# Performance work log

Measured on AMD Instinct MI355X. Metric: run time of the kernel, lower is better.

The kernel has to match this reference:

```python
import jax, jax.numpy as jnp
import numpy as np

NUM_HEADS = 8
BN_EPS = 1e-5


def _conv3x3(x, w, B, N, s):
    # x: (B, N, 3*s*s). Torch loops conv2d per batch element; equivalent to one
    # conv over the flattened (B*N, 3, s, s) batch.
    xi = x.reshape(B * N, 3, s, s)
    y = jax.lax.conv_general_dilated(
        xi, w, window_strides=(1, 1), padding='SAME',
        dimension_numbers=('NCHW', 'OIHW', 'NCHW'))
    return y.reshape(B, N, 3 * s * s)


def setup_inputs() -> dict:
    key = jax.random.key(0)
    ks = jax.random.split(key, 8)
    B, N, C, s = 4, 1024, 768, 16
    H = NUM_HEADS
    q = jax.random.normal(ks[0], (B, N, C), jnp.float32)
    k = jax.random.normal(ks[1], (B, N, C), jnp.float32)
    v = jax.random.normal(ks[2], (B, N, C), jnp.float32)
    qw = jax.random.normal(ks[3], (3, 3, 3, 3), jnp.float32) * 0.1
    kw = jax.random.normal(ks[4], (3, 3, 3, 3), jnp.float32) * 0.1
    vw = jax.random.normal(ks[5], (3, 3, 3, 3), jnp.float32) * 0.1
    rw = jax.random.normal(ks[6], (H, H), jnp.float32) * 0.3  # Conv2d(H,H,1,1) weight
    rb = jnp.zeros((H,), jnp.float32)
    bn_gamma = jnp.ones((H,), jnp.float32)
    bn_beta = jnp.zeros((H,), jnp.float32)
    pw = jax.random.normal(ks[7], (C, C), jnp.float32) * 0.02
    pb = jnp.zeros((C,), jnp.float32)
    return dict(q=q, k=k, v=v, qw=qw, kw=kw, vw=vw, rw=rw, rb=rb,
                bn_gamma=bn_gamma, bn_beta=bn_beta, pw=pw, pb=pb)


def reference(q, k, v, qw, kw, vw, rw, rb, bn_gamma, bn_beta, pw, pb):
    B, N, C = q.shape
    H = NUM_HEADS
    d = C // H
    s = int(np.sqrt(C // 3))
    scale = d ** -0.5
    # conv-projected q/k/v, back to (B, N, C)
    qc = _conv3x3(q, qw, B, N, s)
    kc = _conv3x3(k, kw, B, N, s)
    vc = _conv3x3(v, vw, B, N, s)
    # split heads: (B, H, N, d)
    qh = qc.reshape(B, N, H, d).transpose(0, 2, 1, 3)
    kh = kc.reshape(B, N, H, d).transpose(0, 2, 1, 3)
    vh = vc.reshape(B, N, H, d).transpose(0, 2, 1, 3)
    attn = jax.nn.softmax(jnp.einsum('bhnd,bhmd->bhnm', qh, kh) * scale, axis=-1)
    # re-attention: 1x1 cross-head conv + BatchNorm2d(H) in eval mode
    # (running_mean=0, running_var=1); reatten_scale = 1.0
    attn = jnp.einsum('bhnm,gh->bgnm', attn, rw) + rb[None, :, None, None]
    attn = attn * (bn_gamma / jnp.sqrt(1.0 + BN_EPS))[None, :, None, None] \
           + bn_beta[None, :, None, None]
    x = jnp.einsum('bhnm,bhmd->bhnd', attn, vh)
    x = x.transpose(0, 2, 1, 3).reshape(B, N, C)
    return x @ pw.T + pb
```

## Files before the change

kernel.cpp:

```cpp
#include <hip/hip_runtime.h>
#include <hip/hip_bf16.h>
#include <math.h>

#define B 4
#define N 1024
#define C 768
#define H 8
#define D 96

typedef _Float16 half8 __attribute__((ext_vector_type(8)));
typedef _Float16 half4 __attribute__((ext_vector_type(4)));
typedef float f32x4 __attribute__((ext_vector_type(4)));

#define BN_RSQ 0.9999950000374997f
#define QK_SCALE 0.10206207261596577f

__global__ __launch_bounds__(256) void conv_tok(const float* __restrict__ x,
                                                const float* __restrict__ w,
                                                _Float16* __restrict__ out) {
    __shared__ float sx[768];
    __shared__ float sw[81];
    int t = blockIdx.x;
    const float* xt = x + (size_t)t * 768;
    int tid = threadIdx.x;
    sx[tid]       = xt[tid];
    sx[tid + 256] = xt[tid + 256];
    sx[tid + 512] = xt[tid + 512];
    if (tid < 81) sw[tid] = w[tid];
    __syncthreads();
    int i = tid >> 4, j = tid & 15;
    float acc0 = 0.f, acc1 = 0.f, acc2 = 0.f;
    #pragma unroll
    for (int c = 0; c < 3; ++c) {
        #pragma unroll
        for (int di = 0; di < 3; ++di) {
            int ii = i + di - 1;
            if (ii < 0 || ii > 15) continue;
            #pragma unroll
            for (int dj = 0; dj < 3; ++dj) {
                int jj = j + dj - 1;
                if (jj < 0 || jj > 15) continue;
                float xv = sx[c * 256 + ii * 16 + jj];
                acc0 += xv * sw[(0 * 3 + c) * 9 + di * 3 + dj];
                acc1 += xv * sw[(1 * 3 + c) * 9 + di * 3 + dj];
                acc2 += xv * sw[(2 * 3 + c) * 9 + di * 3 + dj];
            }
        }
    }
    _Float16* ot = out + (size_t)t * 768;
    ot[0 * 256 + tid] = (_Float16)acc0;
    ot[1 * 256 + tid] = (_Float16)acc1;
    ot[2 * 256 + tid] = (_Float16)acc2;
}

__global__ __launch_bounds__(256) void transpose_v(const _Float16* __restrict__ vcH,
                                                   _Float16* __restrict__ vcT) {
    __shared__ _Float16 tile[64][66];
    int n0 = blockIdx.x * 64, c0 = blockIdx.y * 64, b = blockIdx.z;
    int tid = threadIdx.x;
    for (int i = tid; i < 4096; i += 256) {
        int r = i >> 6, c = i & 63;
        tile[r][c] = vcH[((size_t)(b * N + n0 + r)) * C + c0 + c];
    }
    __syncthreads();
    for (int i = tid; i < 4096; i += 256) {
        int cr = i >> 6, nc = i & 63;
        vcT[((size_t)(b * 768 + c0 + cr)) * N + n0 + nc] = tile[nc][cr];
    }
}

__global__ __launch_bounds__(256) void vsum_part(const _Float16* __restrict__ vcH,
                                                 float* __restrict__ vsum) {
    int col = blockIdx.x * 256 + threadIdx.x;
    int b = col / 768, c = col - b * 768;
    int m0 = blockIdx.y * 64;
    float s = 0.f;
    #pragma unroll 8
    for (int m = 0; m < 64; ++m)
        s += (float)vcH[((size_t)(b * N) + m0 + m) * C + c];
    atomicAdd(&vsum[b * 768 + c], s);
}

__global__ __launch_bounds__(256) void qk_mfma(const _Float16* __restrict__ qcH,
                                               const _Float16* __restrict__ kcH,
                                               _Float16* __restrict__ expS,
                                               float* __restrict__ Lrow) {
    __shared__ _Float16 Qt[128 * 96];
    __shared__ _Float16 Kt[128 * 96];
    const int n0 = blockIdx.x * 128, m0 = blockIdx.y * 128, z = blockIdx.z;
    const int b = z >> 3, h = z & 7;
    const int tid = threadIdx.x;
    const _Float16* qg = qcH + ((size_t)(b * N + n0)) * C + h * D;
    const _Float16* kg = kcH + ((size_t)(b * N + m0)) * C + h * D;
    char* Qb = (char*)Qt;
    char* Kb = (char*)Kt;
    #pragma unroll
    for (int it = 0; it < 6; ++it) {
        int chunk = it * 256 + tid;
        int r = chunk / 12, cc = (chunk - r * 12) * 8;
        half8 qv = *(const half8*)(qg + (size_t)r * C + cc);
        half8 kv = *(const half8*)(kg + (size_t)r * C + cc);
        int off = ((r * 96 + cc) * 2) ^ ((r & 7) << 4);
        *(half8*)(Qb + off) = qv;
        *(half8*)(Kb + off) = kv;
    }
    __syncthreads();
    const int wid = tid >> 6, lane = tid & 63;
    const int wr = wid >> 1, wc = wid & 1;
    const int l15 = lane & 15, l4 = lane >> 4;
    f32x4 acc[4][4] = {};
    #pragma unroll
    for (int ks = 0; ks < 3; ++ks) {
        int k0 = ks * 32 + l4 * 8;
        half8 a[4], bf[4];
        #pragma unroll
        for (int fm = 0; fm < 4; ++fm) {
            int row = wr * 64 + fm * 16 + l15;
            a[fm] = *(half8*)(Qb + (((row * 96 + k0) * 2) ^ ((row & 7) << 4)));
        }
        #pragma unroll
        for (int fn = 0; fn < 4; ++fn) {
            int row = wc * 64 + fn * 16 + l15;
            bf[fn] = *(half8*)(Kb + (((row * 96 + k0) * 2) ^ ((row & 7) << 4)));
        }
        #pragma unroll
        for (int fm = 0; fm < 4; ++fm)
            #pragma unroll
            for (int fn = 0; fn < 4; ++fn)
                acc[fm][fn] = __builtin_amdgcn_mfma_f32_16x16x32_f16(a[fm], bf[fn], acc[fm][fn], 0, 0, 0);
    }
    #pragma unroll
    for (int fm = 0; fm < 4; ++fm) {
        #pragma unroll
        for (int j = 0; j < 4; ++j) {
            int row = n0 + wr * 64 + fm * 16 + l4 * 4 + j;
            float rs = 0.f;
            #pragma unroll
            for (int fn = 0; fn < 4; ++fn) {
                float p = __expf(acc[fm][fn][j] * QK_SCALE);
                rs += p;
                int m = m0 + wc * 64 + fn * 16 + l15;
                expS[((size_t)z * N + row) * N + m] = (_Float16)p;
            }
            rs += __shfl_xor(rs, 1);
            rs += __shfl_xor(rs, 2);
            rs += __shfl_xor(rs, 4);
            rs += __shfl_xor(rs, 8);
            if (l15 == 0) atomicAdd(&Lrow[z * N + row], rs);
        }
    }
}

__global__ __launch_bounds__(512, 2) void pv_fused(const _Float16* __restrict__ expS,
                                                   const float* __restrict__ Lrow,
                                                   const _Float16* __restrict__ vcT,
                                                   const float* __restrict__ rw,
                                                   const float* __restrict__ gamma,
                                                   float* __restrict__ x) {
    __shared__ _Float16 AL[8 * 64 * 32];
    __shared__ _Float16 VL[8 * 96 * 32];
    __shared__ float w2s[64];
    const int n0 = blockIdx.x * 64;
    const int mbase = blockIdx.y * 256;
    const int b = blockIdx.z;
    const int tid = threadIdx.x;
    if (tid < 64) {
        int g = tid >> 3, hh = tid & 7;
        w2s[tid] = gamma[g] * BN_RSQ * rw[g * 8 + hh];
    }
    const int n_t = tid >> 3;
    const int mq = (tid & 7) * 4;
    float IL[8];
    #pragma unroll
    for (int h = 0; h < 8; ++h)
        IL[h] = 1.0f / Lrow[(b * 8 + h) * N + n0 + n_t];
    __syncthreads();
    const int wid = tid >> 6, lane = tid & 63;
    const int l15 = lane & 15, l4 = lane >> 4;
    char* ALb = (char*)AL;
    char* VLb = (char*)VL;
    f32x4 acc[4][6] = {};
    for (int msub = 0; msub < 8; ++msub) {
        const int m0 = mbase + msub * 32;
        half4 sE[8];
        #pragma unroll
        for (int h = 0; h < 8; ++h)
            sE[h] = *(const half4*)(expS + ((size_t)(b * 8 + h) * N + n0 + n_t) * N + m0 + mq);
        half8 vv[6];
        int voff[6];
        #pragma unroll
        for (int it = 0; it < 6; ++it) {
            int q = it * 512 + tid;
            int g = q / 384, r = q - g * 384;
            int d = r >> 2, m4 = (r & 3) * 8;
            vv[it] = *(const half8*)(vcT + ((size_t)(b * 768 + g * 96 + d)) * N + m0 + m4);
            voff[it] = g * 6144 + (((d * 32 + m4) * 2) ^ ((d & 7) << 4));
        }
        f32x4 Pq[8];
        #pragma unroll
        for (int h = 0; h < 8; ++h) {
            #pragma unroll
            for (int i = 0; i < 4; ++i) Pq[h][i] = (float)sE[h][i] * IL[h];
        }
        __syncthreads();
        #pragma unroll
        for (int g = 0; g < 8; ++g) {
            f32x4 v = {};
            #pragma unroll
            for (int h = 0; h < 8; ++h) {
                float wv = w2s[g * 8 + h];
                #pragma unroll
                for (int i = 0; i < 4; ++i) v[i] += wv * Pq[h][i];
            }
            half4 hv;
            #pragma unroll
            for (int i = 0; i < 4; ++i) hv[i] = (_Float16)v[i];
            *(half4*)(ALb + (g * 4096 + (((n_t * 32 + mq) * 2) ^ ((n_t & 7) << 4)))) = hv;
        }
        #pragma unroll
        for (int it = 0; it < 6; ++it)
            *(half8*)(VLb + voff[it]) = vv[it];
        __syncthreads();
        half8 af[4];
        #pragma unroll
        for (int fm = 0; fm < 4; ++fm) {
            int n = fm * 16 + l15;
            af[fm] = *(half8*)(ALb + wid * 4096 + (((n * 32 + l4 * 8) * 2) ^ ((n & 7) << 4)));
        }
        #pragma unroll
        for (int fn = 0; fn < 6; ++fn) {
            int d = fn * 16 + l15;
            half8 bf = *(half8*)(VLb + wid * 6144 + (((d * 32 + l4 * 8) * 2) ^ ((d & 7) << 4)));
            #pragma unroll
            for (int fm = 0; fm < 4; ++fm)
                acc[fm][fn] = __builtin_amdgcn_mfma_f32_16x16x32_f16(af[fm], bf, acc[fm][fn], 0, 0, 0);
        }
    }
    #pragma unroll
    for (int fm = 0; fm < 4; ++fm)
        #pragma unroll
        for (int fn = 0; fn < 6; ++fn)
            #pragma unroll
            for (int j = 0; j < 4; ++j) {
                int n = n0 + fm * 16 + l4 * 4 + j;
                int c = wid * 96 + fn * 16 + l15;
                atomicAdd(&x[((size_t)(b * N + n)) * C + c], acc[fm][fn][j]);
            }
}

__global__ __launch_bounds__(256) void proj_mfma(const float* __restrict__ x,
                                                 const float* __restrict__ vsum,
                                                 const float* __restrict__ pw,
                                                 const float* __restrict__ pb,
                                                 const float* __restrict__ rb,
                                                 const float* __restrict__ gamma,
                                                 const float* __restrict__ beta,
                                                 float* __restrict__ out) {
    __shared__ _Float16 sX[128 * 32];
    __shared__ _Float16 sW[96 * 32];
    const int t0 = blockIdx.x * 128, c0 = blockIdx.y * 96;
    const int b = t0 >> 10;
    const int tid = threadIdx.x;
    const int wid = tid >> 6, lane = tid & 63;
    const int wr = wid >> 1, wc = wid & 1;
    const int l15 = lane & 15, l4 = lane >> 4;
    char* Xb = (char*)sX;
    char* Wb = (char*)sW;
    f32x4 acc[4][3] = {};
    for (int k0 = 0; k0 < 768; k0 += 32) {
        __syncthreads();
        #pragma unroll
        for (int it = 0; it < 4; ++it) {
            int q = it * 256 + tid;
            int r = q >> 3, c4 = (q & 7) * 4;
            f32x4 xv = *(const f32x4*)(x + (size_t)(t0 + r) * C + k0 + c4);
            int g = (k0 + c4) / 96;
            float cg = gamma[g] * BN_RSQ * rb[g] + beta[g];
            const f32x4 vs = *(const f32x4*)(vsum + b * 768 + k0 + c4);
            half4 hv;
            #pragma unroll
            for (int i = 0; i < 4; ++i) hv[i] = (_Float16)(xv[i] + cg * vs[i]);
            *(half4*)(Xb + (((r * 32 + c4) * 2) ^ ((r & 7) << 4))) = hv;
        }
        #pragma unroll
        for (int it = 0; it < 3; ++it) {
            int q = it * 256 + tid;
            int r = q >> 3, c4 = (q & 7) * 4;
            f32x4 wv = *(const f32x4*)(pw + (size_t)(c0 + r) * C + k0 + c4);
            half4 hv;
            #pragma unroll
            for (int i = 0; i < 4; ++i) hv[i] = (_Float16)wv[i];
            *(half4*)(Wb + (((r * 32 + c4) * 2) ^ ((r & 7) << 4))) = hv;
        }
        __syncthreads();
        half8 af[4];
        #pragma unroll
        for (int fm = 0; fm < 4; ++fm) {
            int r = wr * 64 + fm * 16 + l15;
            af[fm] = *(half8*)(Xb + (((r * 32 + l4 * 8) * 2) ^ ((r & 7) << 4)));
        }
        #pragma unroll
        for (int fn = 0; fn < 3; ++fn) {
            int r = wc * 48 + fn * 16 + l15;
            half8 bf = *(half8*)(Wb + (((r * 32 + l4 * 8) * 2) ^ ((r & 7) << 4)));
            #pragma unroll
            for (int fm = 0; fm < 4; ++fm)
                acc[fm][fn] = __builtin_amdgcn_mfma_f32_16x16x32_f16(af[fm], bf, acc[fm][fn], 0, 0, 0);
        }
    }
    #pragma unroll
    for (int fm = 0; fm < 4; ++fm)
        #pragma unroll
        for (int fn = 0; fn < 3; ++fn) {
            int cc = c0 + wc * 48 + fn * 16 + l15;
            float bias = pb[cc];
            #pragma unroll
            for (int j = 0; j < 4; ++j) {
                int t = t0 + wr * 64 + fm * 16 + l4 * 4 + j;
                out[(size_t)t * C + cc] = acc[fm][fn][j] + bias;
            }
        }
}

extern "C" void kernel_launch(void* const* d_in, const int* in_sizes, int n_in,
                              void* d_out, int out_size, void* d_ws, size_t ws_size,
                              hipStream_t stream) {
    const float* q     = (const float*)d_in[0];
    const float* k     = (const float*)d_in[1];
    const float* v     = (const float*)d_in[2];
    const float* qw    = (const float*)d_in[3];
    const float* kw    = (const float*)d_in[4];
    const float* vw    = (const float*)d_in[5];
    const float* rw    = (const float*)d_in[6];
    const float* rb    = (const float*)d_in[7];
    const float* gamma = (const float*)d_in[8];
    const float* beta  = (const float*)d_in[9];
    const float* pw    = (const float*)d_in[10];
    const float* pb    = (const float*)d_in[11];
    float* out = (float*)d_out;

    char* ws = (char*)d_ws;
    _Float16* expS = (_Float16*)ws;
    float*    xacc = (float*)(ws + 67108864);
    _Float16* qcH  = (_Float16*)(ws + 79691776);
    _Float16* kcH  = (_Float16*)(ws + 85983232);
    _Float16* vcH  = (_Float16*)(ws + 92274688);
    _Float16* vcT  = (_Float16*)(ws + 98566144);
    float*    Lrow = (float*)(ws + 104857600);
    float*    vsum = (float*)(ws + 104988672);

    hipMemsetAsync(Lrow, 0, 131072, stream);
    hipMemsetAsync(xacc, 0, 12582912, stream);
    hipMemsetAsync(vsum, 0, 12288, stream);

    conv_tok<<<dim3(B * N), dim3(256), 0, stream>>>(q, qw, qcH);
    conv_tok<<<dim3(B * N), dim3(256), 0, stream>>>(k, kw, kcH);
    conv_tok<<<dim3(B * N), dim3(256), 0, stream>>>(v, vw, vcH);

    transpose_v<<<dim3(16, 12, B), dim3(256), 0, stream>>>(vcH, vcT);
    vsum_part<<<dim3(12, 16), dim3(256), 0, stream>>>(vcH, vsum);

    qk_mfma<<<dim3(8, 8, 8 * B), dim3(256), 0, stream>>>(qcH, kcH, expS, Lrow);

    pv_fused<<<dim3(16, 4, B), dim3(512), 0, stream>>>(expS, Lrow, vcT, rw, gamma, xacc);

    proj_mfma<<<dim3(32, 8), dim3(256), 0, stream>>>(xacc, vsum, pw, pb, rb, gamma, beta, out);
}
```

Measured before the change: 268.3 us.

## Stage expS through LDS for coalesced stores; read V fragments directly from global

```diff
diff --git a/kernel.cpp b/kernel.cpp
--- a/kernel.cpp
+++ b/kernel.cpp
@@ -69,31 +69,35 @@
     }
 }
 
-__global__ __launch_bounds__(256) void vsum_part(const _Float16* __restrict__ vcH,
-                                                 float* __restrict__ vsum) {
-    int col = blockIdx.x * 256 + threadIdx.x;
-    int b = col / 768, c = col - b * 768;
-    int m0 = blockIdx.y * 64;
+__global__ __launch_bounds__(256) void vsum_row(const _Float16* __restrict__ vcT,
+                                                float* __restrict__ vsum) {
+    int row = blockIdx.x * 4 + (threadIdx.x >> 6);
+    int lane = threadIdx.x & 63;
+    const _Float16* p = vcT + (size_t)row * N;
     float s = 0.f;
-    #pragma unroll 8
-    for (int m = 0; m < 64; ++m)
-        s += (float)vcH[((size_t)(b * N) + m0 + m) * C + c];
-    atomicAdd(&vsum[b * 768 + c], s);
+    #pragma unroll
+    for (int it = 0; it < 2; ++it) {
+        half8 v = *(const half8*)(p + (it * 64 + lane) * 8);
+        #pragma unroll
+        for (int i = 0; i < 8; ++i) s += (float)v[i];
+    }
+    #pragma unroll
+    for (int off = 1; off < 64; off <<= 1) s += __shfl_xor(s, off);
+    if (lane == 0) vsum[row] = s;
 }
 
 __global__ __launch_bounds__(256) void qk_mfma(const _Float16* __restrict__ qcH,
                                                const _Float16* __restrict__ kcH,
                                                _Float16* __restrict__ expS,
                                                float* __restrict__ Lrow) {
-    __shared__ _Float16 Qt[128 * 96];
-    __shared__ _Float16 Kt[128 * 96];
+    __shared__ __align__(16) char smem[49152];
+    char* Qb = smem;
+    char* Kb = smem + 24576;
     const int n0 = blockIdx.x * 128, m0 = blockIdx.y * 128, z = blockIdx.z;
     const int b = z >> 3, h = z & 7;
     const int tid = threadIdx.x;
     const _Float16* qg = qcH + ((size_t)(b * N + n0)) * C + h * D;
     const _Float16* kg = kcH + ((size_t)(b * N + m0)) * C + h * D;
-    char* Qb = (char*)Qt;
-    char* Kb = (char*)Kt;
     #pragma unroll
     for (int it = 0; it < 6; ++it) {
         int chunk = it * 256 + tid;
@@ -129,25 +133,35 @@
             for (int fn = 0; fn < 4; ++fn)
                 acc[fm][fn] = __builtin_amdgcn_mfma_f32_16x16x32_f16(a[fm], bf[fn], acc[fm][fn], 0, 0, 0);
     }
+    __syncthreads();
     #pragma unroll
     for (int fm = 0; fm < 4; ++fm) {
         #pragma unroll
         for (int j = 0; j < 4; ++j) {
-            int row = n0 + wr * 64 + fm * 16 + l4 * 4 + j;
+            int row = wr * 64 + fm * 16 + l4 * 4 + j;
             float rs = 0.f;
             #pragma unroll
             for (int fn = 0; fn < 4; ++fn) {
                 float p = __expf(acc[fm][fn][j] * QK_SCALE);
                 rs += p;
-                int m = m0 + wc * 64 + fn * 16 + l15;
-                expS[((size_t)z * N + row) * N + m] = (_Float16)p;
+                int col = wc * 64 + fn * 16 + l15;
+                *(_Float16*)(smem + (row * 136 + col) * 2) = (_Float16)p;
             }
             rs += __shfl_xor(rs, 1);
             rs += __shfl_xor(rs, 2);
             rs += __shfl_xor(rs, 4);
             rs += __shfl_xor(rs, 8);
-            if (l15 == 0) atomicAdd(&Lrow[z * N + row], rs);
-        }
+            if (l15 == 0) atomicAdd(&Lrow[z * N + n0 + row], rs);
+        }
+    }
+    __syncthreads();
+    _Float16* eg = expS + ((size_t)z * N + n0) * N + m0;
+    #pragma unroll
+    for (int it = 0; it < 8; ++it) {
+        int q2 = it * 256 + tid;
+        int row = q2 >> 4, col8 = (q2 & 15) * 8;
+        half8 v = *(half8*)(smem + (row * 136 + col8) * 2);
+        *(half8*)(eg + (size_t)row * N + col8) = v;
     }
 }
 
@@ -158,7 +172,6 @@
                                                    const float* __restrict__ gamma,
                                                    float* __restrict__ x) {
     __shared__ _Float16 AL[8 * 64 * 32];
-    __shared__ _Float16 VL[8 * 96 * 32];
     __shared__ float w2s[64];
     const int n0 = blockIdx.x * 64;
     const int mbase = blockIdx.y * 256;
@@ -173,12 +186,12 @@
     float IL[8];
     #pragma unroll
     for (int h = 0; h < 8; ++h)
-        IL[h] = 1.0f / Lrow[(b * 8 + h) * N + n0 + n_t];
+        IL[h] = 1.0f / Lrow[(size_t)(b * 8 + h) * N + n0 + n_t];
     __syncthreads();
     const int wid = tid >> 6, lane = tid & 63;
     const int l15 = lane & 15, l4 = lane >> 4;
     char* ALb = (char*)AL;
-    char* VLb = (char*)VL;
+    const _Float16* vgbase = vcT + (size_t)(b * 768 + wid * 96) * N;
     f32x4 acc[4][6] = {};
     for (int msub = 0; msub < 8; ++msub) {
         const int m0 = mbase + msub * 32;
@@ -186,16 +199,6 @@
         #pragma unroll
         for (int h = 0; h < 8; ++h)
             sE[h] = *(const half4*)(expS + ((size_t)(b * 8 + h) * N + n0 + n_t) * N + m0 + mq);
-        half8 vv[6];
-        int voff[6];
-        #pragma unroll
-        for (int it = 0; it < 6; ++it) {
-            int q = it * 512 + tid;
-            int g = q / 384, r = q - g * 384;
-            int d = r >> 2, m4 = (r & 3) * 8;
-            vv[it] = *(const half8*)(vcT + ((size_t)(b * 768 + g * 96 + d)) * N + m0 + m4);
-            voff[it] = g * 6144 + (((d * 32 + m4) * 2) ^ ((d & 7) << 4));
-        }
         f32x4 Pq[8];
         #pragma unroll
         for (int h = 0; h < 8; ++h) {
@@ -217,9 +220,6 @@
             for (int i = 0; i < 4; ++i) hv[i] = (_Float16)v[i];
             *(half4*)(ALb + (g * 4096 + (((n_t * 32 + mq) * 2) ^ ((n_t & 7) << 4)))) = hv;
         }
-        #pragma unroll
-        for (int it = 0; it < 6; ++it)
-            *(half8*)(VLb + voff[it]) = vv[it];
         __syncthreads();
         half8 af[4];
         #pragma unroll
@@ -230,7 +230,7 @@
         #pragma unroll
         for (int fn = 0; fn < 6; ++fn) {
             int d = fn * 16 + l15;
-            half8 bf = *(half8*)(VLb + wid * 6144 + (((d * 32 + l4 * 8) * 2) ^ ((d & 7) << 4)));
+            half8 bf = *(const half8*)(vgbase + (size_t)d * N + m0 + l4 * 8);
             #pragma unroll
             for (int fm = 0; fm < 4; ++fm)
                 acc[fm][fn] = __builtin_amdgcn_mfma_f32_16x16x32_f16(af[fm], bf, acc[fm][fn], 0, 0, 0);
@@ -351,14 +351,13 @@
 
     hipMemsetAsync(Lrow, 0, 131072, stream);
     hipMemsetAsync(xacc, 0, 12582912, stream);
-    hipMemsetAsync(vsum, 0, 12288, stream);
 
     conv_tok<<<dim3(B * N), dim3(256), 0, stream>>>(q, qw, qcH);
     conv_tok<<<dim3(B * N), dim3(256), 0, stream>>>(k, kw, kcH);
     conv_tok<<<dim3(B * N), dim3(256), 0, stream>>>(v, vw, vcH);
 
     transpose_v<<<dim3(16, 12, B), dim3(256), 0, stream>>>(vcH, vcT);
-    vsum_part<<<dim3(12, 16), dim3(256), 0, stream>>>(vcH, vsum);
+    vsum_row<<<dim3(768), dim3(256), 0, stream>>>(vcT, vsum);
 
     qk_mfma<<<dim3(8, 8, 8 * B), dim3(256), 0, stream>>>(qcH, kcH, expS, Lrow);
 
```

After: 262.4 us. -2.2%, faster.
